# Kernel optimization log

Measured on AMD Instinct MI355X. Metric: run time of the kernel, lower is better.

Reference implementation:

```python
import jax, jax.numpy as jnp
import numpy as np
import math

S, B, E, H = 2048, 2, 1024, 16
D = E // H
LN_EPS = 1e-5


def setup_inputs() -> dict:
    key = jax.random.key(0)
    ks = jax.random.split(key, 8)
    src = jax.random.normal(ks[0], (S, B, E), dtype=jnp.float32)
    # causal attention mask: 1 = attend, 0 = masked
    src_mask = jnp.tril(jnp.ones((S, S), dtype=jnp.int32))
    in_proj_w = jax.random.normal(ks[1], (2 * E, E), dtype=jnp.float32) * 0.02
    in_proj_b = jnp.zeros((2 * E,), dtype=jnp.float32)
    out_proj_w = jax.random.normal(ks[2], (E, E), dtype=jnp.float32) * 0.02
    out_proj_b = jnp.zeros((E,), dtype=jnp.float32)
    ln_g = jnp.ones((E,), dtype=jnp.float32)
    ln_b = jnp.zeros((E,), dtype=jnp.float32)
    return {"src": src, "src_mask": src_mask, "in_proj_w": in_proj_w,
            "in_proj_b": in_proj_b, "out_proj_w": out_proj_w,
            "out_proj_b": out_proj_b, "ln_g": ln_g, "ln_b": ln_b}


def _layernorm(x, g, b):
    mu = jnp.mean(x, axis=-1, keepdims=True)
    var = jnp.mean(jnp.square(x - mu), axis=-1, keepdims=True)
    return (x - mu) * jax.lax.rsqrt(var + LN_EPS) * g + b


def reference(src, src_mask, in_proj_w, in_proj_b, out_proj_w, out_proj_b, ln_g, ln_b):
    # src: (S, B, E)
    x_norm = _layernorm(src, ln_g, ln_b)
    proj = jax.nn.silu(x_norm @ in_proj_w.T + in_proj_b)     # (S, B, 2E)
    qkv, u = jnp.split(proj, 2, axis=-1)                     # each (S, B, E)
    qkv = qkv.reshape(S, B, H, D)                            # q = k = v = qkv
    # scores: (B, H, S_q, S_k)
    scores = jnp.einsum('sbhd,tbhd->bhst', qkv, qkv) / math.sqrt(D)
    # torch does masked_fill(-inf) then silu; silu(-inf) -> 0 in the limit,
    # which is the intended semantics (masked positions contribute nothing).
    weights = jnp.where(src_mask[None, None, :, :] == 0, 0.0, jax.nn.silu(scores))
    # attn_dropout is identity at eval
    attn = jnp.einsum('bhst,tbhd->sbhd', weights, qkv).reshape(S, B, E)
    gated = attn * u
    out = src + (gated @ out_proj_w.T + out_proj_b)          # out_dropout = identity
    return out
```

## Files before the change

### kernel.cpp

```cpp
#include <hip/hip_runtime.h>


typedef __attribute__((ext_vector_type(8))) short  short8;
typedef __attribute__((ext_vector_type(4))) float  floatx4;
typedef __attribute__((ext_vector_type(4))) float  fvec4;
typedef __attribute__((ext_vector_type(4))) unsigned short usvec4;
typedef __attribute__((ext_vector_type(4))) int    intx4;

__device__ __forceinline__ unsigned short f2b(float f) {
  unsigned u = __builtin_bit_cast(unsigned, f);
  u += 0x7FFFu + ((u >> 16) & 1u);
  return (unsigned short)(u >> 16);
}
__device__ __forceinline__ float b2f(unsigned short h) {
  unsigned u = ((unsigned)h) << 16;
  return __builtin_bit_cast(float, u);
}
__device__ __forceinline__ float silu_f(float x) {
  float e = __builtin_amdgcn_exp2f(-1.44269504f * x);
  return x * __builtin_amdgcn_rcpf(1.f + e);
}
__device__ __forceinline__ void async_copy16(void* lds, const void* g) {
  __builtin_amdgcn_global_load_lds(
      (__attribute__((address_space(1))) void*)(g),
      (__attribute__((address_space(3))) void*)(lds), 16, 0, 0);
}

__global__ void cvt_bf16(const float* __restrict__ s1, unsigned short* __restrict__ d1,
                         const float* __restrict__ s2, unsigned short* __restrict__ d2,
                         int n1, int ntot) {
  int i = blockIdx.x * 256 + threadIdx.x;
  if (i >= ntot) return;
  const float* s; unsigned short* d; int j;
  if (i < n1) { s = s1; d = d1; j = i; } else { s = s2; d = d2; j = i - n1; }
  fvec4 v = ((const fvec4*)s)[j];
  usvec4 o = { f2b(v.x), f2b(v.y), f2b(v.z), f2b(v.w) };
  ((usvec4*)d)[j] = o;
}

__global__ __launch_bounds__(256) void ln_kernel(
    const float* __restrict__ x, const float* __restrict__ g,
    const float* __restrict__ b, unsigned short* __restrict__ xn) {
  const int lane = threadIdx.x & 63;
  const int row = blockIdx.x * 4 + (threadIdx.x >> 6);
  const fvec4* xr = (const fvec4*)(x + (long)row * 1024);
  fvec4 v[4];
  float s = 0.f, s2 = 0.f;
  #pragma unroll
  for (int c = 0; c < 4; ++c) {
    v[c] = xr[lane + 64 * c];
    s  += v[c].x + v[c].y + v[c].z + v[c].w;
    s2 += v[c].x*v[c].x + v[c].y*v[c].y + v[c].z*v[c].z + v[c].w*v[c].w;
  }
  #pragma unroll
  for (int off = 32; off; off >>= 1) { s += __shfl_xor(s, off); s2 += __shfl_xor(s2, off); }
  float mu  = s * (1.f / 1024.f);
  float var = s2 * (1.f / 1024.f) - mu * mu;
  float rs  = rsqrtf(var + 1e-5f);
  usvec4* outr = (usvec4*)(xn + (long)row * 1024);
  #pragma unroll
  for (int c = 0; c < 4; ++c) {
    fvec4 gg = ((const fvec4*)g)[lane + 64 * c];
    fvec4 bb = ((const fvec4*)b)[lane + 64 * c];
    usvec4 o = { f2b((v[c].x - mu) * rs * gg.x + bb.x),
                 f2b((v[c].y - mu) * rs * gg.y + bb.y),
                 f2b((v[c].z - mu) * rs * gg.z + bb.z),
                 f2b((v[c].w - mu) * rs * gg.w + bb.w) };
    outr[lane + 64 * c] = o;
  }
}

__global__ __launch_bounds__(256, 2) void gemm_in(
    const unsigned short* __restrict__ A, const unsigned short* __restrict__ Bw,
    const float* __restrict__ bias,
    unsigned short* __restrict__ out0, unsigned short* __restrict__ out1) {
  __shared__ __align__(16) unsigned short sA[2][128 * 32];
  __shared__ __align__(16) unsigned short sB[2][128 * 32];
  const int t = threadIdx.x;
  const int lane = t & 63, l15 = lane & 15, quad = lane >> 4;
  const int w = t >> 6, wm = w >> 1, wn = w & 1;
  const int m0 = blockIdx.y * 128, n0 = blockIdx.x * 128;
  const int K = 1024;

  floatx4 acc[4][4];
  const floatx4 z4 = {0.f, 0.f, 0.f, 0.f};
  #pragma unroll
  for (int i = 0; i < 4; i++)
    #pragma unroll
    for (int j = 0; j < 4; j++) acc[i][j] = z4;

  const int srow = t >> 2, scol = (t & 3) << 3;
  for (int kt = 0; kt < 16; ++kt) {
    const int k0 = kt << 6;
    __syncthreads();
    #pragma unroll
    for (int h = 0; h < 2; ++h) {
      #pragma unroll
      for (int c = 0; c < 2; ++c) {
        int slot = c * 256 + t;
        int row = slot >> 2, col = (slot & 3) << 3;
        async_copy16(&sA[h][slot * 8], &A[(m0 + row) * K + k0 + h * 32 + col]);
        async_copy16(&sB[h][slot * 8], &Bw[(n0 + row) * K + k0 + h * 32 + col]);
      }
    }
    __syncthreads();
    #pragma unroll
    for (int h = 0; h < 2; ++h) {
      short8 af[4], bf[4];
      #pragma unroll
      for (int mr = 0; mr < 4; mr++)
        af[mr] = *(const short8*)&sA[h][(wm * 64 + mr * 16 + l15) * 32 + quad * 8];
      #pragma unroll
      for (int nr = 0; nr < 4; nr++)
        bf[nr] = *(const short8*)&sB[h][(wn * 64 + nr * 16 + l15) * 32 + quad * 8];
      #pragma unroll
      for (int mr = 0; mr < 4; mr++)
        #pragma unroll
        for (int nr = 0; nr < 4; nr++)
          acc[mr][nr] = __builtin_amdgcn_mfma_f32_16x16x32_bf16(af[mr], bf[nr], acc[mr][nr], 0, 0, 0);
    }
  }
  (void)srow; (void)scol;

  #pragma unroll
  for (int mr = 0; mr < 4; mr++) {
    int gm0 = m0 + wm * 64 + mr * 16 + quad * 4;
    #pragma unroll
    for (int nr = 0; nr < 4; nr++) {
      int gn = n0 + wn * 64 + nr * 16 + l15;
      float bv = bias[gn];
      unsigned short* dst = (gn < 1024) ? (out0 + gn) : (out1 + gn - 1024);
      #pragma unroll
      for (int r = 0; r < 4; r++) {
        float v = acc[mr][nr][r] + bv;
        dst[(long)(gm0 + r) * 1024] = f2b(silu_f(v));
      }
    }
  }
}

__global__ __launch_bounds__(256, 2) void gemm_out(
    const unsigned short* __restrict__ A, const unsigned short* __restrict__ Bw,
    const float* __restrict__ bias, const float* __restrict__ src,
    float* __restrict__ outf) {
  __shared__ __align__(16) unsigned short sA[2][128 * 32];
  __shared__ __align__(16) unsigned short sB[2][64 * 32];
  const int t = threadIdx.x;
  const int lane = t & 63, l15 = lane & 15, quad = lane >> 4;
  const int w = t >> 6;
  const int m0 = blockIdx.y * 128, n0 = blockIdx.x * 64;

  floatx4 acc[2][4];
  const floatx4 z4 = {0.f, 0.f, 0.f, 0.f};
  #pragma unroll
  for (int i = 0; i < 2; i++)
    #pragma unroll
    for (int j = 0; j < 4; j++) acc[i][j] = z4;

  for (int kt = 0; kt < 16; ++kt) {
    const int k0 = kt << 6;
    __syncthreads();
    #pragma unroll
    for (int h = 0; h < 2; ++h) {
      #pragma unroll
      for (int c = 0; c < 2; ++c) {
        int slot = c * 256 + t;
        int row = slot >> 2, col = (slot & 3) << 3;
        async_copy16(&sA[h][slot * 8], &A[(m0 + row) * 1024 + k0 + h * 32 + col]);
      }
      { int row = t >> 2, col = (t & 3) << 3;
        async_copy16(&sB[h][t * 8], &Bw[(n0 + row) * 1024 + k0 + h * 32 + col]); }
    }
    __syncthreads();
    #pragma unroll
    for (int h = 0; h < 2; ++h) {
      short8 af[2], bf[4];
      #pragma unroll
      for (int mr = 0; mr < 2; mr++)
        af[mr] = *(const short8*)&sA[h][(w * 32 + mr * 16 + l15) * 32 + quad * 8];
      #pragma unroll
      for (int nr = 0; nr < 4; nr++)
        bf[nr] = *(const short8*)&sB[h][(nr * 16 + l15) * 32 + quad * 8];
      #pragma unroll
      for (int mr = 0; mr < 2; mr++)
        #pragma unroll
        for (int nr = 0; nr < 4; nr++)
          acc[mr][nr] = __builtin_amdgcn_mfma_f32_16x16x32_bf16(af[mr], bf[nr], acc[mr][nr], 0, 0, 0);
    }
  }

  #pragma unroll
  for (int mr = 0; mr < 2; mr++) {
    int gm0 = m0 + w * 32 + mr * 16 + quad * 4;
    #pragma unroll
    for (int nr = 0; nr < 4; nr++) {
      int gn = n0 + nr * 16 + l15;
      float bv = bias[gn];
      #pragma unroll
      for (int r = 0; r < 4; r++) {
        long idx = (long)(gm0 + r) * 1024 + gn;
        outf[idx] = acc[mr][nr][r] + bv + src[idx];
      }
    }
  }
}

#define SKS 72
#define SVS 136
__device__ __forceinline__ void write_kv(unsigned short* sKp, unsigned short* sVp,
                                         const short8* kv, int rg, int dg, int swz0) {
  #pragma unroll
  for (int i = 0; i < 4; ++i)
    *(short8*)&sKp[(rg * 4 + i) * SKS + dg * 8] = kv[i];
  intx4 k0 = __builtin_bit_cast(intx4, kv[0]);
  intx4 k1 = __builtin_bit_cast(intx4, kv[1]);
  intx4 k2 = __builtin_bit_cast(intx4, kv[2]);
  intx4 k3 = __builtin_bit_cast(intx4, kv[3]);
  #pragma unroll
  for (int jj = 0; jj < 4; ++jj) {
    unsigned lo = __builtin_amdgcn_perm((unsigned)k1[jj], (unsigned)k0[jj], 0x05040100u);
    unsigned hi = __builtin_amdgcn_perm((unsigned)k3[jj], (unsigned)k2[jj], 0x05040100u);
    int j = 2 * jj, d = dg * 8 + j;
    int gsw = (swz0 + j) & 15;
    *(unsigned long long*)&sVp[d * SVS + gsw * 8 + (rg & 1) * 4] =
        (unsigned long long)lo | ((unsigned long long)hi << 32);
    lo = __builtin_amdgcn_perm((unsigned)k1[jj], (unsigned)k0[jj], 0x07060302u);
    hi = __builtin_amdgcn_perm((unsigned)k3[jj], (unsigned)k2[jj], 0x07060302u);
    j = 2 * jj + 1; d = dg * 8 + j;
    gsw = (swz0 + j) & 15;
    *(unsigned long long*)&sVp[d * SVS + gsw * 8 + (rg & 1) * 4] =
        (unsigned long long)lo | ((unsigned long long)hi << 32);
  }
}

__global__ __launch_bounds__(256, 2) void attn_kernel(
    const unsigned short* __restrict__ qkv, const unsigned short* __restrict__ u,
    unsigned short* __restrict__ gated) {
  __shared__ __align__(16) unsigned char smem[18432 + 2 * 17408];
  unsigned short* sK   = (unsigned short*)smem;
  unsigned short* sVt0 = (unsigned short*)(smem + 18432);
  unsigned short* sVt1 = (unsigned short*)(smem + 18432 + 17408);
  unsigned short* sQ   = sVt1;
  float*          sR   = (float*)smem;

  const int t = threadIdx.x, lane = t & 63, l15 = lane & 15, quad = lane >> 4;
  const int w = t >> 6;
  const int pair = blockIdx.x >> 5, bh = blockIdx.x & 31;
  const int b = bh >> 4, h = bh & 15;
  const long base = (long)b * 1024 + h * 64;
  const int rg = t >> 3, dg = t & 7;
  const int swz0 = (rg >> 1) + dg;
  const int addr_lo = 4 * (l15 + 32 * (quad & 1));
  const int addr_hi = addr_lo + 64;
  const bool qhi = quad >= 2;
  const int vswz = w * 4 + quad + (l15 & 7) + (l15 >> 3);
  const floatx4 z4 = {0.f, 0.f, 0.f, 0.f};

  for (int half = 0; half < 2; ++half) {
    const int qi = half ? (31 - pair) : pair;
    const int q0 = qi * 64;
    const int nkt = (qi >> 1) + 1;

    if (half) __syncthreads();
    #pragma unroll
    for (int c = 0; c < 2; ++c) {
      int slot = c * 256 + t, row = slot >> 3, cg = slot & 7;
      *(short8*)&sQ[row * SKS + cg * 8] =
          *(const short8*)&qkv[base + (long)(q0 + row) * 2048 + cg * 8];
    }
    __syncthreads();
    short8 qf[4][2];
    #pragma unroll
    for (int nt = 0; nt < 4; nt++)
      #pragma unroll
      for (int ks = 0; ks < 2; ks++)
        qf[nt][ks] = *(const short8*)&sQ[(nt * 16 + l15) * SKS + ks * 32 + quad * 8];
    short8 kv[4];
    #pragma unroll
    for (int i = 0; i < 4; ++i)
      kv[i] = *(const short8*)&qkv[base + (long)(rg * 4 + i) * 2048 + dg * 8];
    write_kv(sK, sVt0, kv, rg, dg, swz0);

    floatx4 oacc[4][4];
    #pragma unroll
    for (int i = 0; i < 4; i++)
      #pragma unroll
      for (int j = 0; j < 4; j++) oacc[i][j] = z4;

    for (int kt = 0; kt < nkt; ++kt) {
      unsigned short* sVtC = (kt & 1) ? sVt1 : sVt0;
      unsigned short* sVtN = (kt & 1) ? sVt0 : sVt1;
      __syncthreads();
      const bool more = (kt + 1 < nkt);
      if (more) {
        const long nb = base + (long)((kt + 1) * 128) * 2048;
        #pragma unroll
        for (int i = 0; i < 4; ++i)
          kv[i] = *(const short8*)&qkv[nb + (long)(rg * 4 + i) * 2048 + dg * 8];
      }
      short8 kf[2][2];
      #pragma unroll
      for (int mt = 0; mt < 2; mt++)
        #pragma unroll
        for (int ks = 0; ks < 2; ks++)
          kf[mt][ks] = *(const short8*)&sK[(w * 32 + mt * 16 + l15) * SKS + ks * 32 + quad * 8];
      __syncthreads();
      floatx4 sacc[2][4];
      #pragma unroll
      for (int i = 0; i < 2; i++)
        #pragma unroll
        for (int j = 0; j < 4; j++) sacc[i][j] = z4;
      #pragma unroll
      for (int ks = 0; ks < 2; ++ks)
        #pragma unroll
        for (int mt = 0; mt < 2; mt++)
          #pragma unroll
          for (int nt = 0; nt < 4; nt++)
            sacc[mt][nt] = __builtin_amdgcn_mfma_f32_16x16x32_bf16(
                kf[mt][ks], qf[nt][ks], sacc[mt][nt], 0, 0, 0);
      const bool diag = (kt == nkt - 1);
      const int tw = kt * 128 + w * 32;
      unsigned p0[2][4], p1[2][4];
      #pragma unroll
      for (int mt = 0; mt < 2; mt++)
        #pragma unroll
        for (int nt = 0; nt < 4; nt++) {
          float v[4];
          if (diag) {
            int qq = q0 + nt * 16 + l15;
            #pragma unroll
            for (int r = 0; r < 4; r++) {
              int tt = tw + mt * 16 + quad * 4 + r;
              float x = silu_f(sacc[mt][nt][r] * 0.125f);
              v[r] = (qq < tt) ? 0.f : x;
            }
          } else {
            #pragma unroll
            for (int r = 0; r < 4; r++) v[r] = silu_f(sacc[mt][nt][r] * 0.125f);
          }
          p0[mt][nt] = __builtin_amdgcn_perm(__builtin_bit_cast(unsigned, v[1]),
                                             __builtin_bit_cast(unsigned, v[0]), 0x07060302u);
          p1[mt][nt] = __builtin_amdgcn_perm(__builtin_bit_cast(unsigned, v[3]),
                                             __builtin_bit_cast(unsigned, v[2]), 0x07060302u);
        }
      short8 vb[4];
      #pragma unroll
      for (int dt = 0; dt < 4; dt++)
        vb[dt] = *(const short8*)&sVtC[(dt * 16 + l15) * SVS + ((vswz + 2 * dt) & 15) * 8];
      #pragma unroll
      for (int qt = 0; qt < 4; qt++) {
        intx4 pa;
        #pragma unroll
        for (int jj = 0; jj < 4; jj++) {
          int addr = (jj >> 1) ? addr_hi : addr_lo;
          int lo, hi;
          if (jj & 1) {
            lo = __builtin_amdgcn_ds_bpermute(addr, (int)p1[0][qt]);
            hi = __builtin_amdgcn_ds_bpermute(addr, (int)p1[1][qt]);
          } else {
            lo = __builtin_amdgcn_ds_bpermute(addr, (int)p0[0][qt]);
            hi = __builtin_amdgcn_ds_bpermute(addr, (int)p0[1][qt]);
          }
          pa[jj] = qhi ? hi : lo;
        }
        short8 paf = __builtin_bit_cast(short8, pa);
        #pragma unroll
        for (int dt = 0; dt < 4; dt++)
          oacc[qt][dt] = __builtin_amdgcn_mfma_f32_16x16x32_bf16(paf, vb[dt], oacc[qt][dt], 0, 0, 0);
      }
      if (more) write_kv(sK, sVtN, kv, rg, dg, swz0);
    }

    __syncthreads();
    float* plane = sR + (w & 1) * 4352;
    if (w < 2) {
      #pragma unroll
      for (int qt = 0; qt < 4; qt++)
        #pragma unroll
        for (int dt = 0; dt < 4; dt++)
          #pragma unroll
          for (int r = 0; r < 4; r++)
            plane[(qt * 16 + quad * 4 + r) * 68 + dt * 16 + l15] = oacc[qt][dt][r];
    }
    __syncthreads();
    if (w >= 2) {
      #pragma unroll
      for (int qt = 0; qt < 4; qt++)
        #pragma unroll
        for (int dt = 0; dt < 4; dt++)
          #pragma unroll
          for (int r = 0; r < 4; r++)
            plane[(qt * 16 + quad * 4 + r) * 68 + dt * 16 + l15] += oacc[qt][dt][r];
    }
    __syncthreads();
    {
      const int erow = t >> 2, edg = t & 3;
      const long grow = (long)(q0 + erow) * 2048 + base + edg * 16;
      short8 u0 = *(const short8*)&u[grow];
      short8 u1 = *(const short8*)&u[grow + 8];
      const float* r0p = sR + erow * 68 + edg * 16;
      const float* r1p = r0p + 4352;
      float o[16];
      #pragma unroll
      for (int c = 0; c < 4; c++) {
        fvec4 a = ((const fvec4*)r0p)[c];
        fvec4 bsum = ((const fvec4*)r1p)[c];
        o[4*c+0] = a.x + bsum.x; o[4*c+1] = a.y + bsum.y;
        o[4*c+2] = a.z + bsum.z; o[4*c+3] = a.w + bsum.w;
      }
      short8 g0, g1;
      #pragma unroll
      for (int j = 0; j < 8; ++j) {
        g0[j] = (short)f2b(o[j]     * b2f((unsigned short)u0[j]));
        g1[j] = (short)f2b(o[j + 8] * b2f((unsigned short)u1[j]));
      }
      *(short8*)&gated[grow]     = g0;
      *(short8*)&gated[grow + 8] = g1;
    }
  }
}

extern "C" void kernel_launch(void* const* d_in, const int* in_sizes, int n_in,
                              void* d_out, int out_size, void* d_ws, size_t ws_size,
                              hipStream_t stream) {
  const float* src = (const float*)d_in[0];
  const float* w1  = (const float*)d_in[2];
  const float* b1  = (const float*)d_in[3];
  const float* w2  = (const float*)d_in[4];
  const float* b2  = (const float*)d_in[5];
  const float* lng = (const float*)d_in[6];
  const float* lnb = (const float*)d_in[7];
  float* out = (float*)d_out;

  char* ws = (char*)d_ws;
  unsigned short* xn    = (unsigned short*)(ws + 0);
  unsigned short* qkv   = (unsigned short*)(ws + 8388608);
  unsigned short* uu    = (unsigned short*)(ws + 16777216);
  unsigned short* gated = (unsigned short*)(ws + 25165824);
  unsigned short* w1b   = (unsigned short*)(ws + 33554432);
  unsigned short* w2b   = (unsigned short*)(ws + 37748736);

  cvt_bf16<<<3072, 256, 0, stream>>>(w1, w1b, w2, w2b, 524288, 786432);
  ln_kernel<<<1024, 256, 0, stream>>>(src, lng, lnb, xn);
  gemm_in<<<dim3(16, 32), 256, 0, stream>>>(xn, w1b, b1, qkv, uu);
  attn_kernel<<<512, 256, 0, stream>>>(qkv, uu, gated);
  gemm_out<<<dim3(16, 32), 256, 0, stream>>>(gated, w2b, b2, src, out);
}
```

Measured before the change: 187.1 us.

## Fuse weight conversion with layernorm and split attention into two launches

The bf16 weight conversion and the layernorm are merged into one prep kernel, which saves a launch. The attention kernel previously made each block handle a paired short and long query tile in sequence. It now runs two launches of 512 blocks, each block doing one query tile: the first covers the low half of the tiles and the second the high half, again pairing short and long tiles across blocks. The goal is more parallelism and better load balance per block, at the cost of an extra launch and of the Q/KV setup no longer being amortised across the pair.

```diff
diff --git a/kernel.cpp b/kernel.cpp
--- a/kernel.cpp
+++ b/kernel.cpp
@@ -26,23 +26,23 @@
       (__attribute__((address_space(3))) void*)(lds), 16, 0, 0);
 }
 
-__global__ void cvt_bf16(const float* __restrict__ s1, unsigned short* __restrict__ d1,
-                         const float* __restrict__ s2, unsigned short* __restrict__ d2,
-                         int n1, int ntot) {
-  int i = blockIdx.x * 256 + threadIdx.x;
-  if (i >= ntot) return;
-  const float* s; unsigned short* d; int j;
-  if (i < n1) { s = s1; d = d1; j = i; } else { s = s2; d = d2; j = i - n1; }
-  fvec4 v = ((const fvec4*)s)[j];
-  usvec4 o = { f2b(v.x), f2b(v.y), f2b(v.z), f2b(v.w) };
-  ((usvec4*)d)[j] = o;
-}
-
-__global__ __launch_bounds__(256) void ln_kernel(
+__global__ __launch_bounds__(256) void prep_kernel(
+    const float* __restrict__ w1, unsigned short* __restrict__ w1b,
+    const float* __restrict__ w2, unsigned short* __restrict__ w2b,
     const float* __restrict__ x, const float* __restrict__ g,
     const float* __restrict__ b, unsigned short* __restrict__ xn) {
+  const int blk = blockIdx.x;
+  if (blk < 3072) {
+    int i = blk * 256 + threadIdx.x;
+    const float* s; unsigned short* d; int j;
+    if (i < 524288) { s = w1; d = w1b; j = i; } else { s = w2; d = w2b; j = i - 524288; }
+    fvec4 v = ((const fvec4*)s)[j];
+    usvec4 o = { f2b(v.x), f2b(v.y), f2b(v.z), f2b(v.w) };
+    ((usvec4*)d)[j] = o;
+    return;
+  }
   const int lane = threadIdx.x & 63;
-  const int row = blockIdx.x * 4 + (threadIdx.x >> 6);
+  const int row = (blk - 3072) * 4 + (threadIdx.x >> 6);
   const fvec4* xr = (const fvec4*)(x + (long)row * 1024);
   fvec4 v[4];
   float s = 0.f, s2 = 0.f;
@@ -89,7 +89,6 @@
     #pragma unroll
     for (int j = 0; j < 4; j++) acc[i][j] = z4;
 
-  const int srow = t >> 2, scol = (t & 3) << 3;
   for (int kt = 0; kt < 16; ++kt) {
     const int k0 = kt << 6;
     __syncthreads();
@@ -120,7 +119,6 @@
           acc[mr][nr] = __builtin_amdgcn_mfma_f32_16x16x32_bf16(af[mr], bf[nr], acc[mr][nr], 0, 0, 0);
     }
   }
-  (void)srow; (void)scol;
 
   #pragma unroll
   for (int mr = 0; mr < 4; mr++) {
@@ -233,6 +231,7 @@
   }
 }
 
+template <int MODE>
 __global__ __launch_bounds__(256, 2) void attn_kernel(
     const unsigned short* __restrict__ qkv, const unsigned short* __restrict__ u,
     unsigned short* __restrict__ gated) {
@@ -245,9 +244,14 @@
 
   const int t = threadIdx.x, lane = t & 63, l15 = lane & 15, quad = lane >> 4;
   const int w = t >> 6;
-  const int pair = blockIdx.x >> 5, bh = blockIdx.x & 31;
+  const int bh = blockIdx.x & 31;
+  const int idx = (blockIdx.x >> 5) & 7, hlf = blockIdx.x >> 8;
+  const int qi = (MODE == 0) ? (hlf ? (15 - idx) : idx)
+                             : (hlf ? (31 - idx) : (16 + idx));
   const int b = bh >> 4, h = bh & 15;
   const long base = (long)b * 1024 + h * 64;
+  const int q0 = qi * 64;
+  const int nkt = (qi >> 1) + 1;
   const int rg = t >> 3, dg = t & 7;
   const int swz0 = (rg >> 1) + dg;
   const int addr_lo = 4 * (l15 + 32 * (quad & 1));
@@ -256,167 +260,160 @@
   const int vswz = w * 4 + quad + (l15 & 7) + (l15 >> 3);
   const floatx4 z4 = {0.f, 0.f, 0.f, 0.f};
 
-  for (int half = 0; half < 2; ++half) {
-    const int qi = half ? (31 - pair) : pair;
-    const int q0 = qi * 64;
-    const int nkt = (qi >> 1) + 1;
-
-    if (half) __syncthreads();
-    #pragma unroll
-    for (int c = 0; c < 2; ++c) {
-      int slot = c * 256 + t, row = slot >> 3, cg = slot & 7;
-      *(short8*)&sQ[row * SKS + cg * 8] =
-          *(const short8*)&qkv[base + (long)(q0 + row) * 2048 + cg * 8];
-    }
-    __syncthreads();
-    short8 qf[4][2];
-    #pragma unroll
-    for (int nt = 0; nt < 4; nt++)
+  #pragma unroll
+  for (int c = 0; c < 2; ++c) {
+    int slot = c * 256 + t, row = slot >> 3, cg = slot & 7;
+    *(short8*)&sQ[row * SKS + cg * 8] =
+        *(const short8*)&qkv[base + (long)(q0 + row) * 2048 + cg * 8];
+  }
+  __syncthreads();
+  short8 qf[4][2];
+  #pragma unroll
+  for (int nt = 0; nt < 4; nt++)
+    #pragma unroll
+    for (int ks = 0; ks < 2; ks++)
+      qf[nt][ks] = *(const short8*)&sQ[(nt * 16 + l15) * SKS + ks * 32 + quad * 8];
+  short8 kv[4];
+  #pragma unroll
+  for (int i = 0; i < 4; ++i)
+    kv[i] = *(const short8*)&qkv[base + (long)(rg * 4 + i) * 2048 + dg * 8];
+  write_kv(sK, sVt0, kv, rg, dg, swz0);
+
+  floatx4 oacc[4][4];
+  #pragma unroll
+  for (int i = 0; i < 4; i++)
+    #pragma unroll
+    for (int j = 0; j < 4; j++) oacc[i][j] = z4;
+
+  for (int kt = 0; kt < nkt; ++kt) {
+    unsigned short* sVtC = (kt & 1) ? sVt1 : sVt0;
+    unsigned short* sVtN = (kt & 1) ? sVt0 : sVt1;
+    __syncthreads();
+    const bool more = (kt + 1 < nkt);
+    if (more) {
+      const long nb = base + (long)((kt + 1) * 128) * 2048;
+      #pragma unroll
+      for (int i = 0; i < 4; ++i)
+        kv[i] = *(const short8*)&qkv[nb + (long)(rg * 4 + i) * 2048 + dg * 8];
+    }
+    short8 kf[2][2];
+    #pragma unroll
+    for (int mt = 0; mt < 2; mt++)
       #pragma unroll
       for (int ks = 0; ks < 2; ks++)
-        qf[nt][ks] = *(const short8*)&sQ[(nt * 16 + l15) * SKS + ks * 32 + quad * 8];
-    short8 kv[4];
-    #pragma unroll
-    for (int i = 0; i < 4; ++i)
-      kv[i] = *(const short8*)&qkv[base + (long)(rg * 4 + i) * 2048 + dg * 8];
-    write_kv(sK, sVt0, kv, rg, dg, swz0);
-
-    floatx4 oacc[4][4];
-    #pragma unroll
-    for (int i = 0; i < 4; i++)
-      #pragma unroll
-      for (int j = 0; j < 4; j++) oacc[i][j] = z4;
-
-    for (int kt = 0; kt < nkt; ++kt) {
-      unsigned short* sVtC = (kt & 1) ? sVt1 : sVt0;
-      unsigned short* sVtN = (kt & 1) ? sVt0 : sVt1;
-      __syncthreads();
-      const bool more = (kt + 1 < nkt);
-      if (more) {
-        const long nb = base + (long)((kt + 1) * 128) * 2048;
-        #pragma unroll
-        for (int i = 0; i < 4; ++i)
-          kv[i] = *(const short8*)&qkv[nb + (long)(rg * 4 + i) * 2048 + dg * 8];
-      }
-      short8 kf[2][2];
+        kf[mt][ks] = *(const short8*)&sK[(w * 32 + mt * 16 + l15) * SKS + ks * 32 + quad * 8];
+    __syncthreads();
+    floatx4 sacc[2][4];
+    #pragma unroll
+    for (int i = 0; i < 2; i++)
+      #pragma unroll
+      for (int j = 0; j < 4; j++) sacc[i][j] = z4;
+    #pragma unroll
+    for (int ks = 0; ks < 2; ++ks)
       #pragma unroll
       for (int mt = 0; mt < 2; mt++)
         #pragma unroll
-        for (int ks = 0; ks < 2; ks++)
-          kf[mt][ks] = *(const short8*)&sK[(w * 32 + mt * 16 + l15) * SKS + ks * 32 + quad * 8];
-      __syncthreads();
-      floatx4 sacc[2][4];
-      #pragma unroll
-      for (int i = 0; i < 2; i++)
+        for (int nt = 0; nt < 4; nt++)
+          sacc[mt][nt] = __builtin_amdgcn_mfma_f32_16x16x32_bf16(
+              kf[mt][ks], qf[nt][ks], sacc[mt][nt], 0, 0, 0);
+    const bool diag = (kt == nkt - 1);
+    const int tw = kt * 128 + w * 32;
+    unsigned p0[2][4], p1[2][4];
+    #pragma unroll
+    for (int mt = 0; mt < 2; mt++)
+      #pragma unroll
+      for (int nt = 0; nt < 4; nt++) {
+        float v[4];
+        if (diag) {
+          int qq = q0 + nt * 16 + l15;
+          #pragma unroll
+          for (int r = 0; r < 4; r++) {
+            int tt = tw + mt * 16 + quad * 4 + r;
+            float x = silu_f(sacc[mt][nt][r] * 0.125f);
+            v[r] = (qq < tt) ? 0.f : x;
+          }
+        } else {
+          #pragma unroll
+          for (int r = 0; r < 4; r++) v[r] = silu_f(sacc[mt][nt][r] * 0.125f);
+        }
+        p0[mt][nt] = __builtin_amdgcn_perm(__builtin_bit_cast(unsigned, v[1]),
+                                           __builtin_bit_cast(unsigned, v[0]), 0x07060302u);
+        p1[mt][nt] = __builtin_amdgcn_perm(__builtin_bit_cast(unsigned, v[3]),
+                                           __builtin_bit_cast(unsigned, v[2]), 0x07060302u);
+      }
+    short8 vb[4];
+    #pragma unroll
+    for (int dt = 0; dt < 4; dt++)
+      vb[dt] = *(const short8*)&sVtC[(dt * 16 + l15) * SVS + ((vswz + 2 * dt) & 15) * 8];
+    #pragma unroll
+    for (int qt = 0; qt < 4; qt++) {
+      intx4 pa;
+      #pragma unroll
+      for (int jj = 0; jj < 4; jj++) {
+        int addr = (jj >> 1) ? addr_hi : addr_lo;
+        int lo, hi;
+        if (jj & 1) {
+          lo = __builtin_amdgcn_ds_bpermute(addr, (int)p1[0][qt]);
+          hi = __builtin_amdgcn_ds_bpermute(addr, (int)p1[1][qt]);
+        } else {
+          lo = __builtin_amdgcn_ds_bpermute(addr, (int)p0[0][qt]);
+          hi = __builtin_amdgcn_ds_bpermute(addr, (int)p0[1][qt]);
+        }
+        pa[jj] = qhi ? hi : lo;
+      }
+      short8 paf = __builtin_bit_cast(short8, pa);
+      #pragma unroll
+      for (int dt = 0; dt < 4; dt++)
+        oacc[qt][dt] = __builtin_amdgcn_mfma_f32_16x16x32_bf16(paf, vb[dt], oacc[qt][dt], 0, 0, 0);
+    }
+    if (more) write_kv(sK, sVtN, kv, rg, dg, swz0);
+  }
+
+  __syncthreads();
+  float* plane = sR + (w & 1) * 4352;
+  if (w < 2) {
+    #pragma unroll
+    for (int qt = 0; qt < 4; qt++)
+      #pragma unroll
+      for (int dt = 0; dt < 4; dt++)
         #pragma unroll
-        for (int j = 0; j < 4; j++) sacc[i][j] = z4;
-      #pragma unroll
-      for (int ks = 0; ks < 2; ++ks)
+        for (int r = 0; r < 4; r++)
+          plane[(qt * 16 + quad * 4 + r) * 68 + dt * 16 + l15] = oacc[qt][dt][r];
+  }
+  __syncthreads();
+  if (w >= 2) {
+    #pragma unroll
+    for (int qt = 0; qt < 4; qt++)
+      #pragma unroll
+      for (int dt = 0; dt < 4; dt++)
         #pragma unroll
-        for (int mt = 0; mt < 2; mt++)
-          #pragma unroll
-          for (int nt = 0; nt < 4; nt++)
-            sacc[mt][nt] = __builtin_amdgcn_mfma_f32_16x16x32_bf16(
-                kf[mt][ks], qf[nt][ks], sacc[mt][nt], 0, 0, 0);
-      const bool diag = (kt == nkt - 1);
-      const int tw = kt * 128 + w * 32;
-      unsigned p0[2][4], p1[2][4];
-      #pragma unroll
-      for (int mt = 0; mt < 2; mt++)
-        #pragma unroll
-        for (int nt = 0; nt < 4; nt++) {
-          float v[4];
-          if (diag) {
-            int qq = q0 + nt * 16 + l15;
-            #pragma unroll
-            for (int r = 0; r < 4; r++) {
-              int tt = tw + mt * 16 + quad * 4 + r;
-              float x = silu_f(sacc[mt][nt][r] * 0.125f);
-              v[r] = (qq < tt) ? 0.f : x;
-            }
-          } else {
-            #pragma unroll
-            for (int r = 0; r < 4; r++) v[r] = silu_f(sacc[mt][nt][r] * 0.125f);
-          }
-          p0[mt][nt] = __builtin_amdgcn_perm(__builtin_bit_cast(unsigned, v[1]),
-                                             __builtin_bit_cast(unsigned, v[0]), 0x07060302u);
-          p1[mt][nt] = __builtin_amdgcn_perm(__builtin_bit_cast(unsigned, v[3]),
-                                             __builtin_bit_cast(unsigned, v[2]), 0x07060302u);
-        }
-      short8 vb[4];
-      #pragma unroll
-      for (int dt = 0; dt < 4; dt++)
-        vb[dt] = *(const short8*)&sVtC[(dt * 16 + l15) * SVS + ((vswz + 2 * dt) & 15) * 8];
-      #pragma unroll
-      for (int qt = 0; qt < 4; qt++) {
-        intx4 pa;
-        #pragma unroll
-        for (int jj = 0; jj < 4; jj++) {
-          int addr = (jj >> 1) ? addr_hi : addr_lo;
-          int lo, hi;
-          if (jj & 1) {
-            lo = __builtin_amdgcn_ds_bpermute(addr, (int)p1[0][qt]);
-            hi = __builtin_amdgcn_ds_bpermute(addr, (int)p1[1][qt]);
-          } else {
-            lo = __builtin_amdgcn_ds_bpermute(addr, (int)p0[0][qt]);
-            hi = __builtin_amdgcn_ds_bpermute(addr, (int)p0[1][qt]);
-          }
-          pa[jj] = qhi ? hi : lo;
-        }
-        short8 paf = __builtin_bit_cast(short8, pa);
-        #pragma unroll
-        for (int dt = 0; dt < 4; dt++)
-          oacc[qt][dt] = __builtin_amdgcn_mfma_f32_16x16x32_bf16(paf, vb[dt], oacc[qt][dt], 0, 0, 0);
-      }
-      if (more) write_kv(sK, sVtN, kv, rg, dg, swz0);
-    }
-
-    __syncthreads();
-    float* plane = sR + (w & 1) * 4352;
-    if (w < 2) {
-      #pragma unroll
-      for (int qt = 0; qt < 4; qt++)
-        #pragma unroll
-        for (int dt = 0; dt < 4; dt++)
-          #pragma unroll
-          for (int r = 0; r < 4; r++)
-            plane[(qt * 16 + quad * 4 + r) * 68 + dt * 16 + l15] = oacc[qt][dt][r];
-    }
-    __syncthreads();
-    if (w >= 2) {
-      #pragma unroll
-      for (int qt = 0; qt < 4; qt++)
-        #pragma unroll
-        for (int dt = 0; dt < 4; dt++)
-          #pragma unroll
-          for (int r = 0; r < 4; r++)
-            plane[(qt * 16 + quad * 4 + r) * 68 + dt * 16 + l15] += oacc[qt][dt][r];
-    }
-    __syncthreads();
-    {
-      const int erow = t >> 2, edg = t & 3;
-      const long grow = (long)(q0 + erow) * 2048 + base + edg * 16;
-      short8 u0 = *(const short8*)&u[grow];
-      short8 u1 = *(const short8*)&u[grow + 8];
-      const float* r0p = sR + erow * 68 + edg * 16;
-      const float* r1p = r0p + 4352;
-      float o[16];
-      #pragma unroll
-      for (int c = 0; c < 4; c++) {
-        fvec4 a = ((const fvec4*)r0p)[c];
-        fvec4 bsum = ((const fvec4*)r1p)[c];
-        o[4*c+0] = a.x + bsum.x; o[4*c+1] = a.y + bsum.y;
-        o[4*c+2] = a.z + bsum.z; o[4*c+3] = a.w + bsum.w;
-      }
-      short8 g0, g1;
-      #pragma unroll
-      for (int j = 0; j < 8; ++j) {
-        g0[j] = (short)f2b(o[j]     * b2f((unsigned short)u0[j]));
-        g1[j] = (short)f2b(o[j + 8] * b2f((unsigned short)u1[j]));
-      }
-      *(short8*)&gated[grow]     = g0;
-      *(short8*)&gated[grow + 8] = g1;
-    }
+        for (int r = 0; r < 4; r++)
+          plane[(qt * 16 + quad * 4 + r) * 68 + dt * 16 + l15] += oacc[qt][dt][r];
+  }
+  __syncthreads();
+  {
+    const int erow = t >> 2, edg = t & 3;
+    const long grow = (long)(q0 + erow) * 2048 + base + edg * 16;
+    short8 u0 = *(const short8*)&u[grow];
+    short8 u1 = *(const short8*)&u[grow + 8];
+    const float* r0p = sR + erow * 68 + edg * 16;
+    const float* r1p = r0p + 4352;
+    float o[16];
+    #pragma unroll
+    for (int c = 0; c < 4; c++) {
+      fvec4 a = ((const fvec4*)r0p)[c];
+      fvec4 bsum = ((const fvec4*)r1p)[c];
+      o[4*c+0] = a.x + bsum.x; o[4*c+1] = a.y + bsum.y;
+      o[4*c+2] = a.z + bsum.z; o[4*c+3] = a.w + bsum.w;
+    }
+    short8 g0, g1;
+    #pragma unroll
+    for (int j = 0; j < 8; ++j) {
+      g0[j] = (short)f2b(o[j]     * b2f((unsigned short)u0[j]));
+      g1[j] = (short)f2b(o[j + 8] * b2f((unsigned short)u1[j]));
+    }
+    *(short8*)&gated[grow]     = g0;
+    *(short8*)&gated[grow + 8] = g1;
   }
 }
 
@@ -440,9 +437,9 @@
   unsigned short* w1b   = (unsigned short*)(ws + 33554432);
   unsigned short* w2b   = (unsigned short*)(ws + 37748736);
 
-  cvt_bf16<<<3072, 256, 0, stream>>>(w1, w1b, w2, w2b, 524288, 786432);
-  ln_kernel<<<1024, 256, 0, stream>>>(src, lng, lnb, xn);
+  prep_kernel<<<4096, 256, 0, stream>>>(w1, w1b, w2, w2b, src, lng, lnb, xn);
   gemm_in<<<dim3(16, 32), 256, 0, stream>>>(xn, w1b, b1, qkv, uu);
-  attn_kernel<<<512, 256, 0, stream>>>(qkv, uu, gated);
+  attn_kernel<0><<<512, 256, 0, stream>>>(qkv, uu, gated);
+  attn_kernel<1><<<512, 256, 0, stream>>>(qkv, uu, gated);
   gemm_out<<<dim3(16, 32), 256, 0, stream>>>(gated, w2b, b2, src, out);
 }
```

Result: no change. 190.8 us (+2.0%).
